# Kernel optimization log

Hardware: AMD Instinct MI355X
Metric: run time of the kernel (lower is better)

## Reference

```python
import jax, jax.numpy as jnp
import numpy as np
from jax import lax

B, CIN, COUT, H, W = 4, 256, 256, 64, 64
K = 3  # kernel size
PAD = 1
STRIDE = 1


def setup_inputs() -> dict:
    key = jax.random.key(0)
    k1, k2, k3, k4 = jax.random.split(key, 4)
    x = jax.random.normal(k1, (B, CIN, H, W), dtype=jnp.float32)
    # small offset weights so learned offsets are modest (original init is zeros)
    offset_w = jax.random.normal(k2, (3 * K * K, CIN, K, K), dtype=jnp.float32) * 0.01
    offset_b = jax.random.normal(k3, (3 * K * K,), dtype=jnp.float32) * 0.01
    dcn_w = jax.random.normal(k4, (COUT, CIN, K, K), dtype=jnp.float32) * (1.0 / np.sqrt(CIN * K * K))
    return {"x": x, "offset_w": offset_w, "offset_b": offset_b, "dcn_w": dcn_w}


def _dcnv2(x, offset_w, offset_b, dcn_w):
    b, c, h, w = x.shape
    kk = K * K
    # offset conv (standard 3x3, stride 1, pad 1)
    o = lax.conv_general_dilated(
        x, offset_w, (STRIDE, STRIDE), ((PAD, PAD), (PAD, PAD)),
        dimension_numbers=("NCHW", "OIHW", "NCHW"))
    o = o + offset_b[None, :, None, None]
    ho, wo = o.shape[2], o.shape[3]
    off = o[:, : 2 * kk].reshape(b, kk, 2, ho, wo)  # pairs are (dy, dx)
    dy, dx = off[:, :, 0], off[:, :, 1]             # [b,kk,ho,wo]
    mask = jax.nn.sigmoid(o[:, 2 * kk:])            # [b,kk,ho,wo]

    ki, kj = jnp.meshgrid(jnp.arange(K), jnp.arange(K), indexing="ij")
    ki = ki.reshape(kk).astype(jnp.float32)
    kj = kj.reshape(kk).astype(jnp.float32)
    base_y = (jnp.arange(ho, dtype=jnp.float32) * STRIDE - PAD)[None, None, :, None] + ki[None, :, None, None]
    base_x = (jnp.arange(wo, dtype=jnp.float32) * STRIDE - PAD)[None, None, None, :] + kj[None, :, None, None]
    py = base_y + dy  # [b,kk,ho,wo] sampling y
    px = base_x + dx  # sampling x

    y0 = jnp.floor(py)
    x0 = jnp.floor(px)
    wy = py - y0  # bilinear fractional weights
    wx = px - x0
    y0i = y0.astype(jnp.int32)
    x0i = x0.astype(jnp.int32)

    xT = x.transpose(0, 2, 3, 1)  # [b,h,w,c] for channel-last gathers
    bidx = jnp.arange(b)[:, None, None, None]

    def gather(yi, xi):
        # zero padding outside the image
        valid = (yi >= 0) & (yi < h) & (xi >= 0) & (xi < w)
        yc = jnp.clip(yi, 0, h - 1)
        xc = jnp.clip(xi, 0, w - 1)
        v = xT[bidx, yc, xc]  # [b,kk,ho,wo,c]
        return v * valid[..., None].astype(x.dtype)

    g00 = gather(y0i, x0i)
    g01 = gather(y0i, x0i + 1)
    g10 = gather(y0i + 1, x0i)
    g11 = gather(y0i + 1, x0i + 1)

    wy_ = wy[..., None]
    wx_ = wx[..., None]
    sampled = (g00 * (1 - wy_) * (1 - wx_) + g01 * (1 - wy_) * wx_
               + g10 * wy_ * (1 - wx_) + g11 * wy_ * wx_)
    sampled = sampled * mask[..., None]  # modulation

    wk = dcn_w.reshape(dcn_w.shape[0], c, kk)  # [o,c,kk]
    return jnp.einsum("bkhwc,ock->bohw", sampled, wk)


def reference(x, offset_w, offset_b, dcn_w):
    return _dcnv2(x, offset_w, offset_b, dcn_w)
```

## Files before the change

kernel.cpp:

```cpp
#include <hip/hip_runtime.h>
#include <hip/hip_bf16.h>
#include <stdint.h>
#include <math.h>

#define KDIM 2304

typedef __attribute__((ext_vector_type(8))) short bf16x8;
typedef __attribute__((ext_vector_type(4))) float f32x4;

__device__ inline unsigned short f2bf(float f) {
  union { float f; unsigned int u; } v; v.f = f;
  unsigned int u = v.u;
  unsigned int r = (u + 0x7FFFu + ((u >> 16) & 1u)) >> 16;
  return (unsigned short)r;
}
__device__ inline float bf2f(unsigned short h) {
  union { unsigned int u; float f; } v; v.u = ((unsigned int)h) << 16;
  return v.f;
}

__device__ inline void gl2lds16(const void* g, void* l) {
  __builtin_amdgcn_global_load_lds((const __attribute__((address_space(1))) void*)g,
                                   (__attribute__((address_space(3))) void*)l,
                                   16, 0, 0);
}

__global__ __launch_bounds__(256) void k_prep(const float* __restrict__ x,
                                              unsigned short* __restrict__ xTb,
                                              const float* __restrict__ dcn_w,
                                              const float* __restrict__ offset_w,
                                              unsigned short* __restrict__ Wpk,
                                              unsigned short* __restrict__ Wob,
                                              unsigned short* __restrict__ zp) {
  __shared__ float tile[32][65];
  int bx = (int)blockIdx.x;
  int t = threadIdx.x;
  if (bx < 2048) {
    int pt = bx & 127, ct = (bx >> 7) & 3, b = bx >> 9;
    int p0 = pt * 32, c0 = ct * 64;
    const float* xb = x + ((size_t)b << 20);
#pragma unroll
    for (int i = 0; i < 2; ++i) {
      int idx = t + i * 256;
      int c = idx >> 3, pq = idx & 7;
      float4 v = *(const float4*)(xb + ((size_t)(c0 + c) << 12) + p0 + pq * 4);
      tile[pq * 4 + 0][c] = v.x;
      tile[pq * 4 + 1][c] = v.y;
      tile[pq * 4 + 2][c] = v.z;
      tile[pq * 4 + 3][c] = v.w;
    }
    __syncthreads();
    unsigned short* ob = xTb + ((size_t)b << 20);
#pragma unroll
    for (int i = 0; i < 2; ++i) {
      int idx = t + i * 256;
      int p = idx >> 4, cg = idx & 15;
      ushort4 o;
      o.x = f2bf(tile[p][cg * 4 + 0]);
      o.y = f2bf(tile[p][cg * 4 + 1]);
      o.z = f2bf(tile[p][cg * 4 + 2]);
      o.w = f2bf(tile[p][cg * 4 + 3]);
      *(ushort4*)(ob + (((size_t)(p0 + p)) << 8) + c0 + cg * 4) = o;
    }
  } else {
    int gid = (bx - 2048) * 256 + t;
    const int N1 = 72 * 8192;
    const int N2 = 32 * KDIM;
    if (gid < N1) {
      int j = gid & 7;
      int lane = (gid >> 3) & 63;
      int mb = (gid >> 9) & 15;
      int kc = gid >> 13;
      int row = mb * 16 + (lane & 15);
      int gk = kc * 32 + ((lane >> 4) << 3) + j;
      int c = gk & 255, kidx = gk >> 8;
      Wpk[gid] = f2bf(dcn_w[((size_t)(row * 256 + c)) * 9 + kidx]);
    } else if (gid < N1 + N2) {
      int g = gid - N1;
      int ch = g / KDIM, k = g % KDIM;
      int kidx = k >> 8, c = k & 255;
      Wob[g] = (ch < 27) ? f2bf(offset_w[((size_t)(ch * 256 + c)) * 9 + kidx])
                         : (unsigned short)0;
    } else if (gid < N1 + N2 + 128) {
      zp[gid - N1 - N2] = 0;
    }
  }
}

__global__ __launch_bounds__(256) void k_offs(const unsigned short* __restrict__ xTb,
                                              const unsigned short* __restrict__ Wob,
                                              const unsigned short* __restrict__ zp,
                                              const float* __restrict__ offb,
                                              float* __restrict__ SW) {
  __shared__ unsigned short As[4][32 * 32];
  __shared__ unsigned short Bs[4][32 * 32];
  __shared__ float Os[32][33];
  int t = threadIdx.x;
  int wv = t >> 6, lane = t & 63;
  int bid = (int)blockIdx.x;
  int swz = (bid & 7) * 64 + (bid >> 3);
  int n0 = swz * 32;

  int r0 = (t >> 2) & 31, coff = (t & 3) * 8;
  int rowA = n0 + r0;
  int b_ = rowA >> 12, hw = rowA & 4095, h = hw >> 6, w = hw & 63;
  int rB = ((t - 128) >> 2) & 31;

  f32x4 acc = {};

  auto stage = [&](int kt) {
    int buf = kt & 3;
    int k0 = kt * 32;
    int kidx = k0 >> 8, c0 = k0 & 255;
    if (t < 128) {
      int di = kidx / 3 - 1, dj = kidx % 3 - 1;
      int y = h + di, xx = w + dj;
      const unsigned short* g = (y >= 0 && y < 64 && xx >= 0 && xx < 64)
          ? xTb + (((((size_t)b_) << 12) + (y << 6) + xx) << 8) + c0 + coff
          : zp;
      gl2lds16(g, (char*)As[buf] + wv * 1024);
    } else {
      const unsigned short* gB = Wob + (size_t)rB * KDIM + k0 + coff;
      gl2lds16(gB, (char*)Bs[buf] + (wv - 2) * 1024);
    }
  };

  stage(0); stage(1); stage(2);

  int mf = wv & 1, nf = wv >> 1;
  for (int kt = 0; kt < 72; ++kt) {
    if (kt <= 69)      asm volatile("s_waitcnt vmcnt(2)" ::: "memory");
    else if (kt == 70) asm volatile("s_waitcnt vmcnt(1)" ::: "memory");
    else               asm volatile("s_waitcnt vmcnt(0)" ::: "memory");
    asm volatile("s_barrier" ::: "memory");
    if (kt + 3 < 72) stage(kt + 3);
    int buf = kt & 3;
    bf16x8 aF = *(const bf16x8*)(As[buf] + (mf * 16 + (lane & 15)) * 32 + (lane >> 4) * 8);
    bf16x8 bF = *(const bf16x8*)(Bs[buf] + (nf * 16 + (lane & 15)) * 32 + (lane >> 4) * 8);
    acc = __builtin_amdgcn_mfma_f32_16x16x32_bf16(aF, bF, acc, 0, 0, 0);
  }

  int quad = lane >> 4, cl = lane & 15;
#pragma unroll
  for (int r = 0; r < 4; ++r)
    Os[mf * 16 + quad * 4 + r][nf * 16 + cl] = acc[r];
  __syncthreads();

  for (int item = t; item < 288; item += 256) {
    int bl = item & 31, k = item >> 5;
    int bhw = n0 + bl;
    int h_ = (bhw >> 6) & 63, w_ = bhw & 63;
    float dy = Os[bl][2 * k]     + offb[2 * k];
    float dx = Os[bl][2 * k + 1] + offb[2 * k + 1];
    float mv = Os[bl][18 + k]    + offb[18 + k];
    float mask = 1.0f / (1.0f + expf(-mv));

    float py = (float)(h_ - 1 + k / 3) + dy;
    float px = (float)(w_ - 1 + k % 3) + dx;
    float y0f = floorf(py), x0f = floorf(px);
    float wy = py - y0f, wx = px - x0f;
    int y0 = (int)y0f, x0 = (int)x0f;
    int y1 = y0 + 1, x1 = x0 + 1;

    float vy0 = (y0 >= 0 && y0 < 64) ? 1.f : 0.f;
    float vy1 = (y1 >= 0 && y1 < 64) ? 1.f : 0.f;
    float vx0 = (x0 >= 0 && x0 < 64) ? 1.f : 0.f;
    float vx1 = (x1 >= 0 && x1 < 64) ? 1.f : 0.f;
    int y0c = min(max(y0, 0), 63), y1c = min(max(y1, 0), 63);
    int x0c = min(max(x0, 0), 63), x1c = min(max(x1, 0), 63);

    float4 wv4;
    wv4.x = (1.f - wy) * (1.f - wx) * vy0 * vx0 * mask;
    wv4.y = (1.f - wy) * wx * vy0 * vx1 * mask;
    wv4.z = wy * (1.f - wx) * vy1 * vx0 * mask;
    wv4.w = wy * wx * vy1 * vx1 * mask;
    uint4 ov;
    ov.x = (unsigned)(((y0c << 6) + x0c) << 8);
    ov.y = (unsigned)(((y0c << 6) + x1c) << 8);
    ov.z = (unsigned)(((y1c << 6) + x0c) << 8);
    ov.w = (unsigned)(((y1c << 6) + x1c) << 8);

    float* p = SW + (size_t)(k * 16384 + bhw) * 8;
    *(float4*)p = wv4;
    *(uint4*)(p + 4) = ov;
  }
}

#define PHASE(PH, Q, AF, BUF)                                                  \
  do {                                                                         \
    float s_[8];                                                               \
    _Pragma("unroll")                                                          \
    for (int j_ = 0; j_ < 8; ++j_)                                             \
      s_[j_] = wv4.x * bf2f((unsigned short)Q[0][j_]) +                        \
               wv4.y * bf2f((unsigned short)Q[1][j_]) +                        \
               wv4.z * bf2f((unsigned short)Q[2][j_]) +                        \
               wv4.w * bf2f((unsigned short)Q[3][j_]);                         \
    union { __hip_bfloat162 h2[4]; bf16x8 v; } pk_;                            \
    pk_.h2[0] = __float22bfloat162_rn(make_float2(s_[0], s_[1]));              \
    pk_.h2[1] = __float22bfloat162_rn(make_float2(s_[2], s_[3]));              \
    pk_.h2[2] = __float22bfloat162_rn(make_float2(s_[4], s_[5]));              \
    pk_.h2[3] = __float22bfloat162_rn(make_float2(s_[6], s_[7]));              \
    *(bf16x8*)(&Bs[BUF][s_th][bsw]) = pk_.v;                                   \
    if (((PH) & 3) == 0 && (PH) < 32) {                                        \
      const float* swp_ =                                                      \
          SW + ((size_t)((((PH) >> 2) + 1) * 16384 + n0 + r)) * 8;             \
      wv4n = *(const float4*)swp_;                                             \
      ovn  = *(const uint4*)(swp_ + 4);                                        \
    }                                                                          \
    if ((PH) < 34) {                                                           \
      int kn0_ = 2 * (PH) + 4;                                                 \
      uint4 o_ = (((PH) & 3) >= 2) ? ovn : ov;                                 \
      unsigned c_ = (unsigned)((((kn0_ & 7) + s_th) << 5) + gg * 8);           \
      Q[0] = *(const bf16x8*)(xb + o_.x + c_);                                 \
      Q[1] = *(const bf16x8*)(xb + o_.y + c_);                                 \
      Q[2] = *(const bf16x8*)(xb + o_.z + c_);                                 \
      Q[3] = *(const bf16x8*)(xb + o_.w + c_);                                 \
    }                                                                          \
    asm volatile("s_waitcnt lgkmcnt(0)\n\ts_barrier" ::: "memory");            \
    _Pragma("unroll")                                                          \
    for (int s2_ = 0; s2_ < 2; ++s2_) {                                        \
      bf16x8 bF0_ = *(const bf16x8*)(                                          \
          &Bs[BUF][s2_][(wn * 32 + (lane & 15)) * 56 + (lane >> 4) * 8]);      \
      bf16x8 bF1_ = *(const bf16x8*)(                                          \
          &Bs[BUF][s2_][(wn * 32 + 16 + (lane & 15)) * 56 + (lane >> 4) * 8]); \
      _Pragma("unroll")                                                        \
      for (int i_ = 0; i_ < 4; ++i_) {                                         \
        acc[i_][0] = __builtin_amdgcn_mfma_f32_16x16x32_bf16(                  \
            AF[s2_ * 4 + i_], bF0_, acc[i_][0], 0, 0, 0);                      \
        acc[i_][1] = __builtin_amdgcn_mfma_f32_16x16x32_bf16(                  \
            AF[s2_ * 4 + i_], bF1_, acc[i_][1], 0, 0, 0);                      \
      }                                                                        \
    }                                                                          \
    if ((PH) < 34) {                                                           \
      _Pragma("unroll")                                                        \
      for (int i_ = 0; i_ < 8; ++i_)                                           \
        AF[i_] = *(const bf16x8*)(                                             \
            wpBase + ((size_t)((2 * (PH) + 4 + (i_ >> 2)) * 16 + (i_ & 3))) * 512); \
    }                                                                          \
  } while (0)

__global__ __launch_bounds__(512, 2) void k_fused(const unsigned short* __restrict__ Wpk,
                                                  const unsigned short* __restrict__ xTb,
                                                  const float* __restrict__ SW,
                                                  float* __restrict__ out) {
  __shared__ __align__(16) unsigned short Bs[2][2][64 * 56];
  int t = threadIdx.x;
  int wv = t >> 6, lane = t & 63;
  int wm = wv & 3, wn = wv >> 2;
  int bid = (int)blockIdx.x;
  int swz = (bid & 7) * 32 + (bid >> 3);
  int n0 = swz * 64;
  int b  = n0 >> 12;
  const unsigned short* xb = xTb + ((size_t)b << 20);

  int r = t >> 3;
  int u = t & 7;
  int s_th = u & 1, gg = u >> 1;
  int bsw = r * 56 + gg * 8;

  const unsigned short* wpBase = Wpk + ((size_t)(wm * 4 * 64 + lane)) * 8;

  f32x4 acc[4][2] = {};

  float4 wv4, wv4n; uint4 ov, ovn;
  {
    const float* sw = SW + ((size_t)(n0 + r)) * 8;
    wv4 = *(const float4*)sw;
    ov  = *(const uint4*)(sw + 4);
  }
  wv4n = wv4; ovn = ov;

  bf16x8 qA[4], qB[4];
  bf16x8 aFA[8], aFB[8];

  {
    unsigned cA = (unsigned)((s_th << 5) + gg * 8);
    unsigned cB = (unsigned)(((2 + s_th) << 5) + gg * 8);
    qA[0] = *(const bf16x8*)(xb + ov.x + cA);
    qA[1] = *(const bf16x8*)(xb + ov.y + cA);
    qA[2] = *(const bf16x8*)(xb + ov.z + cA);
    qA[3] = *(const bf16x8*)(xb + ov.w + cA);
    qB[0] = *(const bf16x8*)(xb + ov.x + cB);
    qB[1] = *(const bf16x8*)(xb + ov.y + cB);
    qB[2] = *(const bf16x8*)(xb + ov.z + cB);
    qB[3] = *(const bf16x8*)(xb + ov.w + cB);
#pragma unroll
    for (int i = 0; i < 8; ++i) {
      aFA[i] = *(const bf16x8*)(wpBase + ((size_t)(((i >> 2)) * 16 + (i & 3))) * 512);
      aFB[i] = *(const bf16x8*)(wpBase + ((size_t)((2 + (i >> 2)) * 16 + (i & 3))) * 512);
    }
  }

  for (int ph = 0; ph < 36; ph += 2) {
    PHASE(ph,     qA, aFA, 0);
    PHASE(ph + 1, qB, aFB, 1);
    if ((ph & 3) == 2) { wv4 = wv4n; ov = ovn; }
  }

  int quad = lane >> 4, cl = lane & 15;
  float* ob = out + (((size_t)b) << 20);
#pragma unroll
  for (int i = 0; i < 4; ++i) {
    int mbase = wm * 64 + i * 16 + quad * 4;
#pragma unroll
    for (int j = 0; j < 2; ++j) {
      int hw = (n0 & 4095) + wn * 32 + j * 16 + cl;
      float* op = ob + hw;
#pragma unroll
      for (int rr = 0; rr < 4; ++rr)
        op[((size_t)(mbase + rr)) << 12] = acc[i][j][rr];
    }
  }
}

extern "C" void kernel_launch(void* const* d_in, const int* in_sizes, int n_in,
                              void* d_out, int out_size, void* d_ws, size_t ws_size,
                              hipStream_t stream) {
  const float* x        = (const float*)d_in[0];
  const float* offset_w = (const float*)d_in[1];
  const float* offset_b = (const float*)d_in[2];
  const float* dcn_w    = (const float*)d_in[3];
  float* out = (float*)d_out;

  char* ws = (char*)d_ws;
  size_t off = 0;
  auto carve = [&](size_t bytes) -> void* {
    void* p = ws + off;
    off += (bytes + 255) & ~(size_t)255;
    return p;
  };
  unsigned short* xTb = (unsigned short*)carve(4ull * 64 * 64 * 256 * 2);
  unsigned short* Wpk = (unsigned short*)carve(72ull * 8192 * 2);
  unsigned short* Wob = (unsigned short*)carve(32ull * KDIM * 2);
  unsigned short* zp  = (unsigned short*)carve(256);
  float*          SW  = (float*)carve(9ull * 16384 * 8 * 4);
  (void)ws_size; (void)in_sizes; (void)n_in; (void)out_size;

  const int WPREP_BLOCKS = (72 * 8192 + 32 * KDIM + 128 + 255) / 256;
  k_prep<<<dim3(2048 + WPREP_BLOCKS), 256, 0, stream>>>(
      x, xTb, dcn_w, offset_w, Wpk, Wob, zp);
  k_offs<<<dim3(512), 256, 0, stream>>>(xTb, Wob, zp, offset_b, SW);
  k_fused<<<dim3(256), 512, 0, stream>>>(Wpk, xTb, SW, out);
}
```

Before: 135.6 us.

## Stage sampling tables in LDS and hand-manage global load waits with vmcnt

```diff
diff --git a/kernel.cpp b/kernel.cpp
--- a/kernel.cpp
+++ b/kernel.cpp
@@ -24,6 +24,9 @@
                                    (__attribute__((address_space(3))) void*)l,
                                    16, 0, 0);
 }
+
+#define GLOAD16(dst, ptr) \
+  asm volatile("global_load_dwordx4 %0, %1, off" : "=v"(dst) : "v"(ptr))
 
 __global__ __launch_bounds__(256) void k_prep(const float* __restrict__ x,
                                               unsigned short* __restrict__ xTb,
@@ -186,8 +189,17 @@
   }
 }
 
-#define PHASE(PH, Q, AF, BUF)                                                  \
+#define PHASE(PH, Q, AF, BUF, WB, WM)                                          \
   do {                                                                         \
+    if (((PH) & 3) == 0) {                                                     \
+      int g_ = (PH) >> 2;                                                      \
+      wv4 = *(const float4*)(SWL + (size_t)(g_ * 128 + r * 2) * 4);            \
+      ov  = *(const uint4*)(SWL + (size_t)(g_ * 128 + r * 2 + 1) * 4);         \
+    } else if (((PH) & 3) == 2 && (PH) < 32) {                                 \
+      ov  = *(const uint4*)(SWL + (size_t)((((PH) >> 2) + 1) * 128 + r * 2 + 1) * 4); \
+    }                                                                          \
+    asm volatile("s_waitcnt vmcnt(" #WB ")" ::: "memory");                     \
+    __builtin_amdgcn_sched_barrier(0);                                         \
     float s_[8];                                                               \
     _Pragma("unroll")                                                          \
     for (int j_ = 0; j_ < 8; ++j_)                                             \
@@ -201,22 +213,16 @@
     pk_.h2[2] = __float22bfloat162_rn(make_float2(s_[4], s_[5]));              \
     pk_.h2[3] = __float22bfloat162_rn(make_float2(s_[6], s_[7]));              \
     *(bf16x8*)(&Bs[BUF][s_th][bsw]) = pk_.v;                                   \
-    if (((PH) & 3) == 0 && (PH) < 32) {                                        \
-      const float* swp_ =                                                      \
-          SW + ((size_t)((((PH) >> 2) + 1) * 16384 + n0 + r)) * 8;             \
-      wv4n = *(const float4*)swp_;                                             \
-      ovn  = *(const uint4*)(swp_ + 4);                                        \
-    }                                                                          \
     if ((PH) < 34) {                                                           \
       int kn0_ = 2 * (PH) + 4;                                                 \
-      uint4 o_ = (((PH) & 3) >= 2) ? ovn : ov;                                 \
       unsigned c_ = (unsigned)((((kn0_ & 7) + s_th) << 5) + gg * 8);           \
-      Q[0] = *(const bf16x8*)(xb + o_.x + c_);                                 \
-      Q[1] = *(const bf16x8*)(xb + o_.y + c_);                                 \
-      Q[2] = *(const bf16x8*)(xb + o_.z + c_);                                 \
-      Q[3] = *(const bf16x8*)(xb + o_.w + c_);                                 \
+      GLOAD16(Q[0], xb + ov.x + c_);                                           \
+      GLOAD16(Q[1], xb + ov.y + c_);                                           \
+      GLOAD16(Q[2], xb + ov.z + c_);                                           \
+      GLOAD16(Q[3], xb + ov.w + c_);                                           \
     }                                                                          \
-    asm volatile("s_waitcnt lgkmcnt(0)\n\ts_barrier" ::: "memory");            \
+    asm volatile("s_waitcnt vmcnt(" #WM ") lgkmcnt(0)\n\ts_barrier" ::: "memory"); \
+    __builtin_amdgcn_sched_barrier(0);                                         \
     _Pragma("unroll")                                                          \
     for (int s2_ = 0; s2_ < 2; ++s2_) {                                        \
       bf16x8 bF0_ = *(const bf16x8*)(                                          \
@@ -233,9 +239,11 @@
     }                                                                          \
     if ((PH) < 34) {                                                           \
       _Pragma("unroll")                                                        \
-      for (int i_ = 0; i_ < 8; ++i_)                                           \
-        AF[i_] = *(const bf16x8*)(                                             \
-            wpBase + ((size_t)((2 * (PH) + 4 + (i_ >> 2)) * 16 + (i_ & 3))) * 512); \
+      for (int i_ = 0; i_ < 8; ++i_) {                                         \
+        const unsigned short* ap_ =                                            \
+            wpBase + ((size_t)((2 * (PH) + 4 + (i_ >> 2)) * 16 + (i_ & 3))) * 512; \
+        GLOAD16(AF[i_], ap_);                                                  \
+      }                                                                        \
     }                                                                          \
   } while (0)
 
@@ -244,6 +252,7 @@
                                                   const float* __restrict__ SW,
                                                   float* __restrict__ out) {
   __shared__ __align__(16) unsigned short Bs[2][2][64 * 56];
+  __shared__ __align__(16) float SWL[1152 * 4];
   int t = threadIdx.x;
   int wv = t >> 6, lane = t & 63;
   int wm = wv & 3, wn = wv >> 2;
@@ -262,40 +271,57 @@
 
   f32x4 acc[4][2] = {};
 
-  float4 wv4, wv4n; uint4 ov, ovn;
   {
-    const float* sw = SW + ((size_t)(n0 + r)) * 8;
-    wv4 = *(const float4*)sw;
-    ov  = *(const uint4*)(sw + 4);
-  }
-  wv4n = wv4; ovn = ov;
+#pragma unroll
+    for (int i = 0; i < 3; ++i) {
+      int hs = t + i * 512;
+      if (hs < 1152) {
+        int grp = hs >> 7, row = (hs >> 1) & 63, hh = hs & 1;
+        const float* src = SW + ((size_t)(grp * 16384 + n0 + row)) * 8 + hh * 4;
+        char* dstbase = (char*)SWL + ((size_t)((t & ~63) + i * 512)) * 16;
+        gl2lds16(src, dstbase);
+      }
+    }
+  }
+  asm volatile("s_waitcnt vmcnt(0)" ::: "memory");
+  __builtin_amdgcn_s_barrier();
+
+  float4 wv4; uint4 ov;
+  wv4 = *(const float4*)(SWL + (size_t)(r * 2) * 4);
+  ov  = *(const uint4*)(SWL + (size_t)(r * 2 + 1) * 4);
 
   bf16x8 qA[4], qB[4];
   bf16x8 aFA[8], aFB[8];
 
   {
     unsigned cA = (unsigned)((s_th << 5) + gg * 8);
+    GLOAD16(qA[0], xb + ov.x + cA);
+    GLOAD16(qA[1], xb + ov.y + cA);
+    GLOAD16(qA[2], xb + ov.z + cA);
+    GLOAD16(qA[3], xb + ov.w + cA);
+#pragma unroll
+    for (int i = 0; i < 8; ++i) {
+      const unsigned short* ap = wpBase + ((size_t)(((i >> 2)) * 16 + (i & 3))) * 512;
+      GLOAD16(aFA[i], ap);
+    }
     unsigned cB = (unsigned)(((2 + s_th) << 5) + gg * 8);
-    qA[0] = *(const bf16x8*)(xb + ov.x + cA);
-    qA[1] = *(const bf16x8*)(xb + ov.y + cA);
-    qA[2] = *(const bf16x8*)(xb + ov.z + cA);
-    qA[3] = *(const bf16x8*)(xb + ov.w + cA);
-    qB[0] = *(const bf16x8*)(xb + ov.x + cB);
-    qB[1] = *(const bf16x8*)(xb + ov.y + cB);
-    qB[2] = *(const bf16x8*)(xb + ov.z + cB);
-    qB[3] = *(const bf16x8*)(xb + ov.w + cB);
+    GLOAD16(qB[0], xb + ov.x + cB);
+    GLOAD16(qB[1], xb + ov.y + cB);
+    GLOAD16(qB[2], xb + ov.z + cB);
+    GLOAD16(qB[3], xb + ov.w + cB);
 #pragma unroll
     for (int i = 0; i < 8; ++i) {
-      aFA[i] = *(const bf16x8*)(wpBase + ((size_t)(((i >> 2)) * 16 + (i & 3))) * 512);
-      aFB[i] = *(const bf16x8*)(wpBase + ((size_t)((2 + (i >> 2)) * 16 + (i & 3))) * 512);
-    }
-  }
-
-  for (int ph = 0; ph < 36; ph += 2) {
-    PHASE(ph,     qA, aFA, 0);
-    PHASE(ph + 1, qB, aFB, 1);
-    if ((ph & 3) == 2) { wv4 = wv4n; ov = ovn; }
-  }
+      const unsigned short* ap = wpBase + ((size_t)((2 + (i >> 2)) * 16 + (i & 3))) * 512;
+      GLOAD16(aFB[i], ap);
+    }
+  }
+
+  for (int ph = 0; ph < 34; ph += 2) {
+    PHASE(ph,     qA, aFA, 0, 20, 16);
+    PHASE(ph + 1, qB, aFB, 1, 20, 16);
+  }
+  PHASE(34, qA, aFA, 0, 20, 12);
+  PHASE(35, qB, aFB, 1, 8, 0);
 
   int quad = lane >> 4, cl = lane & 15;
   float* ob = out + (((size_t)b) << 20);
```

After: 131.6 us. 1.03x faster.
